# Kernel optimization log

Measured on AMD Instinct MI355X. Metric: run time of the kernel, lower is better.

## Reference

```python
import jax, jax.numpy as jnp
import numpy as np

N_GENES = 2048   # col_dim: nodes of the PPI graph, feature dim of cols-SAGE
N_CELLS = 4096   # row_dim: nodes of the KNN graph, feature dim of rows-SAGE
E_KNN = 61440
E_PPI = 65536
INTER = 512
EMBD = 128
SLOPE = 0.01       # LeakyReLU default negative_slope
SCALE_PARAM = 3.0  # cols_encoder custom attention scale

_PARAM_SHAPES = [
    ("c0_wl", (N_GENES, N_GENES)), ("c0_wr", (N_GENES, N_GENES)), ("c0_b", (N_GENES,)),
    ("r0_wl", (N_CELLS, N_CELLS)), ("r0_wr", (N_CELLS, N_CELLS)), ("r0_b", (N_CELLS,)),
    ("c1_wl", (N_GENES, N_GENES)), ("c1_wr", (N_GENES, N_GENES)), ("c1_b", (N_GENES,)),
    ("r1_wl", (N_CELLS, N_CELLS)), ("r1_wr", (N_CELLS, N_CELLS)), ("r1_b", (N_CELLS,)),
    ("gr_w", (N_CELLS, INTER)), ("gr_b", (INTER,)),
    ("tr_wq", (INTER, EMBD)), ("tr_bq", (EMBD,)), ("tr_wk", (INTER, EMBD)), ("tr_bk", (EMBD,)),
    ("tr_wv", (INTER, EMBD)), ("tr_bv", (EMBD,)), ("tr_ws", (INTER, EMBD)), ("tr_bs", (EMBD,)),
    ("gc_w", (N_GENES, INTER)), ("gc_b", (INTER,)),
    ("tc_wq", (INTER, EMBD)), ("tc_bq", (EMBD,)), ("tc_wk", (INTER, EMBD)), ("tc_bk", (EMBD,)),
    ("tc_wv", (INTER, EMBD)), ("tc_bv", (EMBD,)), ("tc_ws", (INTER, EMBD)), ("tc_bs", (EMBD,)),
    ("d1_w", (EMBD, INTER)), ("d1_b", (INTER,)),
    ("d2_w", (INTER, INTER)), ("d2_b", (INTER,)),
    ("d3_w", (INTER, N_GENES)), ("d3_b", (N_GENES,)),
]


def setup_inputs() -> dict:
    key = jax.random.key(0)
    ki = iter(jax.random.split(key, 64))
    inp = {
        "x": jax.random.normal(next(ki), (N_GENES, N_CELLS), jnp.float32),
        "knn_edge_index": jax.random.randint(next(ki), (2, E_KNN), 0, N_CELLS, dtype=jnp.int32),
        "ppi_edge_index": jax.random.randint(next(ki), (2, E_PPI), 0, N_GENES, dtype=jnp.int32),
    }
    for name, shape in _PARAM_SHAPES:
        scale = 1.0 / float(np.sqrt(shape[0])) if len(shape) == 2 else 0.01
        inp[name] = jax.random.normal(next(ki), shape, jnp.float32) * scale
    return inp


def _leaky(x):
    return jax.nn.leaky_relu(x, SLOPE)


def _gcn(x, ei, w, b):
    # GCNConv: add self loops, symmetric D^-1/2 (A+I) D^-1/2 normalization
    n = x.shape[0]
    loop = jnp.arange(n, dtype=ei.dtype)
    src = jnp.concatenate([ei[0], loop])
    dst = jnp.concatenate([ei[1], loop])
    deg = jax.ops.segment_sum(jnp.ones(src.shape, x.dtype), dst, n)
    dinv = jnp.where(deg > 0, jax.lax.rsqrt(jnp.maximum(deg, 1.0)), 0.0)
    h = x @ w
    msg = h[src] * (dinv[src] * dinv[dst])[:, None]
    return jax.ops.segment_sum(msg, dst, n) + b


def _sage(x, ei, wl, wr, b):
    # SAGEConv: mean neighbor aggregation -> lin_l, plus root lin_r
    n = x.shape[0]
    src, dst = ei[0], ei[1]
    s = jax.ops.segment_sum(x[src], dst, n)
    cnt = jax.ops.segment_sum(jnp.ones(src.shape, x.dtype), dst, n)
    agg = s / jnp.maximum(cnt, 1.0)[:, None]
    return agg @ wl + x @ wr + b


def _tconv(x, ei, wq, bq, wk, bk, wv, bv, ws, bs, scale_param):
    # TransformerConv (heads=1). scale_param=None -> per-target softmax;
    # otherwise the custom mean/std standardization + sigmoid (TransformerConvReducrLayer).
    n, d = x.shape[0], wq.shape[1]
    q = x @ wq + bq
    k = x @ wk + bk
    v = x @ wv + bv
    src, dst = ei[0], ei[1]
    alpha = jnp.sum(q[dst] * k[src], axis=-1) / jnp.sqrt(jnp.asarray(d, x.dtype))
    if scale_param is None:
        m = jax.ops.segment_max(alpha, dst, n)
        e = jnp.exp(alpha - m[dst])
        z = jax.ops.segment_sum(e, dst, n)
        a = e / jnp.where(z > 0, z, 1.0)[dst]
    else:
        mu = jnp.mean(alpha)
        sd = jnp.std(alpha, ddof=1)  # torch.std is unbiased
        a = jax.nn.sigmoid((alpha - mu) / ((1.0 / scale_param) * sd))
    out = jax.ops.segment_sum(a[:, None] * v[src], dst, n)
    return out + x @ ws + bs  # root skip (lin_skip)


def reference(x, knn_edge_index, ppi_edge_index,
              c0_wl, c0_wr, c0_b, r0_wl, r0_wr, r0_b,
              c1_wl, c1_wr, c1_b, r1_wl, r1_wr, r1_b,
              gr_w, gr_b, tr_wq, tr_bq, tr_wk, tr_bk, tr_wv, tr_bv, tr_ws, tr_bs,
              gc_w, gc_b, tc_wq, tc_bq, tc_wk, tc_bk, tc_wv, tc_bv, tc_ws, tc_bs,
              d1_w, d1_b, d2_w, d2_b, d3_w, d3_b):
    # dropout layers are identity at inference
    emb = x  # [genes, cells]
    for (cwl, cwr, cb, rwl, rwr, rb) in [
        (c0_wl, c0_wr, c0_b, r0_wl, r0_wr, r0_b),
        (c1_wl, c1_wr, c1_b, r1_wl, r1_wr, r1_b),
    ]:
        emb = _leaky(_sage(emb.T, knn_edge_index, cwl, cwr, cb)).T  # cells graph
        emb = _leaky(_sage(emb, ppi_edge_index, rwl, rwr, rb))      # genes graph
    # rows encoder: GCN + TransformerConv (softmax attention) over PPI graph
    hr = _leaky(_gcn(emb, ppi_edge_index, gr_w, gr_b))
    emb_rows = _tconv(hr, ppi_edge_index, tr_wq, tr_bq, tr_wk, tr_bk,
                      tr_wv, tr_bv, tr_ws, tr_bs, None)
    # cols encoder: GCN + reducer TransformerConv (sigmoid-standardized attention) over KNN graph
    hc = _leaky(_gcn(emb.T, knn_edge_index, gc_w, gc_b))
    emb_cols = _tconv(hc, knn_edge_index, tc_wq, tc_bq, tc_wk, tc_bk,
                      tc_wv, tc_bv, tc_ws, tc_bs, SCALE_PARAM)
    # feature decoder MLP
    h = jax.nn.relu(emb_cols @ d1_w + d1_b)
    h = jax.nn.relu(h @ d2_w + d2_b)
    out_features = h @ d3_w + d3_b
    return (emb_rows, emb_cols, out_features)
```

## Files before the change

kernel.cpp:

```cpp
#include <hip/hip_runtime.h>
#include <math.h>

#define NG 2048
#define NC 4096
#define EKNN 61440
#define EPPI 65536
#define NJMAX 14

typedef __attribute__((ext_vector_type(8))) short short8v;
typedef __attribute__((ext_vector_type(4))) float f32x4;
typedef unsigned short ushort_t;

static inline int cdiv(int a, int b) { return (a + b - 1) / b; }

__device__ __forceinline__ unsigned short f2b(float f) {
    union { float f; unsigned int i; } v; v.f = f;
    unsigned int r = v.i + 0x7FFFu + ((v.i >> 16) & 1u);
    return (unsigned short)(r >> 16);
}
__device__ __forceinline__ float bl(unsigned int u) { union { unsigned int i; float f; } v; v.i = u << 16; return v.f; }
__device__ __forceinline__ float bh(unsigned int u) { union { unsigned int i; float f; } v; v.i = u & 0xFFFF0000u; return v.f; }
__device__ __forceinline__ unsigned int pk2(float a, float b) { return (unsigned int)f2b(a) | ((unsigned int)f2b(b) << 16); }

__device__ __forceinline__ int xcd_swz_id() {
    const int nwg = gridDim.x * gridDim.y;
    const int orig = blockIdx.y * gridDim.x + blockIdx.x;
    const int q = nwg >> 3, r = nwg & 7;
    const int xcd = orig & 7, off = orig >> 3;
    return (xcd < r ? xcd * (q + 1) : r * (q + 1) + (xcd - r) * q) + off;
}

#define GLOAD_LDS16(gp, lp) __builtin_amdgcn_global_load_lds( \
    (const __attribute__((address_space(1))) void*)(gp),      \
    (__attribute__((address_space(3))) void*)(lp), 16, 0, 0)

struct TJobs {
    const void* in[NJMAX];
    ushort_t* out[NJMAX];
    int R[NJMAX], C[NJMAX], start[NJMAX], type[NJMAX];
    int n;
    int nGather;
};

template<int ACT, bool BIAS, bool OBF>
__global__ __launch_bounds__(256)
void gemm_bf16(const ushort_t* __restrict__ A,
               const ushort_t* __restrict__ Bt,
               const float* __restrict__ bias,
               float* __restrict__ Cf, ushort_t* __restrict__ Cb,
               int M, int N, int K) {
    __shared__ ushort_t lds[2][2][128 * 32];
    const int tid = threadIdx.x;
    const int lane = tid & 63, wv = tid >> 6;
    const int wm = wv >> 1, wn = wv & 1;
    const int swzid = xcd_swz_id();
    const int bm = (swzid / gridDim.x) << 7, bn = (swzid % gridDim.x) << 7;

    const ushort_t* gA = A + (size_t)bm * K;
    const ushort_t* gB = Bt + (size_t)bn * K;
    const int rsub = lane >> 2;
    const int qsw  = (lane & 3) ^ ((lane >> 3) & 3);
    const int KT = K >> 5;

    f32x4 acc[4][4];
    #pragma unroll
    for (int i = 0; i < 4; ++i)
        #pragma unroll
        for (int j = 0; j < 4; ++j) acc[i][j] = (f32x4){0.f, 0.f, 0.f, 0.f};

    auto stage = [&](int buf, int k0) {
        #pragma unroll
        for (int t = 0; t < 2; ++t) {
            const int br = (wv * 2 + t) * 16;
            GLOAD_LDS16(gA + (size_t)(br + rsub) * K + k0 + qsw * 8, &lds[buf][0][br * 32]);
            GLOAD_LDS16(gB + (size_t)(br + rsub) * K + k0 + qsw * 8, &lds[buf][1][br * 32]);
        }
    };
    const int rl = lane & 15, kg = lane >> 4;
    const int swr = (kg ^ ((rl >> 1) & 3)) * 8;

    stage(0, 0);
    int buf = 0;
    for (int kt = 0; kt < KT; ++kt) {
        __syncthreads();
        if (kt + 1 < KT) stage(buf ^ 1, (kt + 1) << 5);
        short8v a[4], b[4];
        #pragma unroll
        for (int mi = 0; mi < 4; ++mi)
            a[mi] = *(const short8v*)&lds[buf][0][(wm * 64 + mi * 16 + rl) * 32 + swr];
        #pragma unroll
        for (int ni = 0; ni < 4; ++ni)
            b[ni] = *(const short8v*)&lds[buf][1][(wn * 64 + ni * 16 + rl) * 32 + swr];
        #pragma unroll
        for (int mi = 0; mi < 4; ++mi)
            #pragma unroll
            for (int ni = 0; ni < 4; ++ni)
                acc[mi][ni] = __builtin_amdgcn_mfma_f32_16x16x32_bf16(a[mi], b[ni], acc[mi][ni], 0, 0, 0);
        buf ^= 1;
    }
    const int colL = lane & 15, rq = lane >> 4;
    #pragma unroll
    for (int mi = 0; mi < 4; ++mi) {
        const int row0 = bm + wm * 64 + mi * 16 + rq * 4;
        #pragma unroll
        for (int ni = 0; ni < 4; ++ni) {
            const int col = bn + wn * 64 + ni * 16 + colL;
            float bv = 0.f;
            if (BIAS) bv = bias[col];
            #pragma unroll
            for (int r = 0; r < 4; ++r) {
                const size_t off = (size_t)(row0 + r) * N + col;
                float v = acc[mi][ni][r];
                if (BIAS) v += bv;
                if (ACT == 2) v = fmaxf(v, 0.f);
                if (OBF) Cb[off] = f2b(v); else Cf[off] = v;
            }
        }
    }
}

template<bool BIAS, bool OBF>
__global__ __launch_bounds__(256)
void gemm2_bf16(const ushort_t* __restrict__ A0, const ushort_t* __restrict__ Bt0,
                const float* __restrict__ bias0, float* __restrict__ Cf0, ushort_t* __restrict__ Cb0,
                int N0, int K0, int nx0, int nb0,
                const ushort_t* __restrict__ A1, const ushort_t* __restrict__ Bt1,
                const float* __restrict__ bias1, float* __restrict__ Cf1, ushort_t* __restrict__ Cb1,
                int N1, int K1, int nx1) {
    __shared__ ushort_t lds[2][2][128 * 32];
    const int bid = blockIdx.x;
    const bool p1 = bid >= nb0;
    const int lbid = p1 ? bid - nb0 : bid;
    const ushort_t* A = p1 ? A1 : A0;
    const ushort_t* Bt = p1 ? Bt1 : Bt0;
    const float* bias = p1 ? bias1 : bias0;
    float* Cf = p1 ? Cf1 : Cf0;
    ushort_t* Cb = p1 ? Cb1 : Cb0;
    const int N = p1 ? N1 : N0;
    const int K = p1 ? K1 : K0;
    const int nx = p1 ? nx1 : nx0;
    const int bn = (lbid % nx) << 7, bm = (lbid / nx) << 7;

    const int tid = threadIdx.x;
    const int lane = tid & 63, wv = tid >> 6;
    const int wm = wv >> 1, wn = wv & 1;
    const ushort_t* gA = A + (size_t)bm * K;
    const ushort_t* gB = Bt + (size_t)bn * K;
    const int rsub = lane >> 2;
    const int qsw  = (lane & 3) ^ ((lane >> 3) & 3);
    const int KT = K >> 5;

    f32x4 acc[4][4];
    #pragma unroll
    for (int i = 0; i < 4; ++i)
        #pragma unroll
        for (int j = 0; j < 4; ++j) acc[i][j] = (f32x4){0.f, 0.f, 0.f, 0.f};

    auto stage = [&](int buf, int k0) {
        #pragma unroll
        for (int t = 0; t < 2; ++t) {
            const int br = (wv * 2 + t) * 16;
            GLOAD_LDS16(gA + (size_t)(br + rsub) * K + k0 + qsw * 8, &lds[buf][0][br * 32]);
            GLOAD_LDS16(gB + (size_t)(br + rsub) * K + k0 + qsw * 8, &lds[buf][1][br * 32]);
        }
    };
    const int rl = lane & 15, kg = lane >> 4;
    const int swr = (kg ^ ((rl >> 1) & 3)) * 8;

    stage(0, 0);
    int buf = 0;
    for (int kt = 0; kt < KT; ++kt) {
        __syncthreads();
        if (kt + 1 < KT) stage(buf ^ 1, (kt + 1) << 5);
        short8v a[4], b[4];
        #pragma unroll
        for (int mi = 0; mi < 4; ++mi)
            a[mi] = *(const short8v*)&lds[buf][0][(wm * 64 + mi * 16 + rl) * 32 + swr];
        #pragma unroll
        for (int ni = 0; ni < 4; ++ni)
            b[ni] = *(const short8v*)&lds[buf][1][(wn * 64 + ni * 16 + rl) * 32 + swr];
        #pragma unroll
        for (int mi = 0; mi < 4; ++mi)
            #pragma unroll
            for (int ni = 0; ni < 4; ++ni)
                acc[mi][ni] = __builtin_amdgcn_mfma_f32_16x16x32_bf16(a[mi], b[ni], acc[mi][ni], 0, 0, 0);
        buf ^= 1;
    }
    const int colL = lane & 15, rq = lane >> 4;
    #pragma unroll
    for (int mi = 0; mi < 4; ++mi) {
        const int row0 = bm + wm * 64 + mi * 16 + rq * 4;
        #pragma unroll
        for (int ni = 0; ni < 4; ++ni) {
            const int col = bn + wn * 64 + ni * 16 + colL;
            float bv = 0.f;
            if (BIAS) bv = bias[col];
            #pragma unroll
            for (int r = 0; r < 4; ++r) {
                const size_t off = (size_t)(row0 + r) * N + col;
                float v = acc[mi][ni][r];
                if (BIAS) v += bv;
                if (OBF) Cb[off] = f2b(v); else Cf[off] = v;
            }
        }
    }
}

__global__ __launch_bounds__(256)
void gemm_sage(const ushort_t* __restrict__ A0, const ushort_t* __restrict__ B0t,
               const ushort_t* __restrict__ A1, const ushort_t* __restrict__ B1t,
               const float* __restrict__ bias, ushort_t* __restrict__ Cb,
               int M, int N, int K) {
    __shared__ ushort_t lds[2][2][128 * 32];
    const int tid = threadIdx.x;
    const int lane = tid & 63, wv = tid >> 6;
    const int wm = wv >> 1, wn = wv & 1;
    const int swzid = xcd_swz_id();
    const int bm = (swzid / gridDim.x) << 7, bn = (swzid % gridDim.x) << 7;

    const ushort_t* gA0 = A0 + (size_t)bm * K;
    const ushort_t* gB0 = B0t + (size_t)bn * K;
    const ushort_t* gA1 = A1 + (size_t)bm * K;
    const ushort_t* gB1 = B1t + (size_t)bn * K;
    const int rsub = lane >> 2;
    const int qsw  = (lane & 3) ^ ((lane >> 3) & 3);
    const int KT = K >> 5;

    f32x4 acc[4][4];
    #pragma unroll
    for (int i = 0; i < 4; ++i)
        #pragma unroll
        for (int j = 0; j < 4; ++j) acc[i][j] = (f32x4){0.f, 0.f, 0.f, 0.f};

    auto stage = [&](int buf, int kt) {
        const int half = kt >= KT;
        const int k0 = (half ? (kt - KT) : kt) << 5;
        const ushort_t* sA = half ? gA1 : gA0;
        const ushort_t* sB = half ? gB1 : gB0;
        #pragma unroll
        for (int t = 0; t < 2; ++t) {
            const int br = (wv * 2 + t) * 16;
            GLOAD_LDS16(sA + (size_t)(br + rsub) * K + k0 + qsw * 8, &lds[buf][0][br * 32]);
            GLOAD_LDS16(sB + (size_t)(br + rsub) * K + k0 + qsw * 8, &lds[buf][1][br * 32]);
        }
    };
    const int rl = lane & 15, kg = lane >> 4;
    const int swr = (kg ^ ((rl >> 1) & 3)) * 8;

    stage(0, 0);
    int buf = 0;
    const int KT2 = KT * 2;
    for (int kt = 0; kt < KT2; ++kt) {
        __syncthreads();
        if (kt + 1 < KT2) stage(buf ^ 1, kt + 1);
        short8v a[4], b[4];
        #pragma unroll
        for (int mi = 0; mi < 4; ++mi)
            a[mi] = *(const short8v*)&lds[buf][0][(wm * 64 + mi * 16 + rl) * 32 + swr];
        #pragma unroll
        for (int ni = 0; ni < 4; ++ni)
            b[ni] = *(const short8v*)&lds[buf][1][(wn * 64 + ni * 16 + rl) * 32 + swr];
        #pragma unroll
        for (int mi = 0; mi < 4; ++mi)
            #pragma unroll
            for (int ni = 0; ni < 4; ++ni)
                acc[mi][ni] = __builtin_amdgcn_mfma_f32_16x16x32_bf16(a[mi], b[ni], acc[mi][ni], 0, 0, 0);
        buf ^= 1;
    }
    const int colL = lane & 15, rq = lane >> 4;
    #pragma unroll
    for (int mi = 0; mi < 4; ++mi) {
        const int row0 = bm + wm * 64 + mi * 16 + rq * 4;
        float bz[4];
        #pragma unroll
        for (int r = 0; r < 4; ++r) bz[r] = bias[row0 + r];
        #pragma unroll
        for (int ni = 0; ni < 4; ++ni) {
            const int col = bn + wn * 64 + ni * 16 + colL;
            #pragma unroll
            for (int r = 0; r < 4; ++r) {
                float v = acc[mi][ni][r] + bz[r];
                v = v > 0.f ? v : 0.01f * v;
                Cb[(size_t)(row0 + r) * N + col] = f2b(v);
            }
        }
    }
}

template<int NS>
__global__ __launch_bounds__(256)
void gather_tr(const int* __restrict__ rowptr, const int* __restrict__ srcs,
               const ushort_t* __restrict__ x, ushort_t* __restrict__ xout,
               TJobs jobs) {
    __shared__ ushort_t shm[64 * 65];
    const int tid = threadIdx.x;
    if ((int)blockIdx.x < jobs.nGather) {
        const int F = NS * 2048;
        const int node = blockIdx.x;
        int* snb = (int*)shm;
        const int beg = rowptr[node], end = rowptr[node + 1];
        float acc[NS][8];
        #pragma unroll
        for (int s = 0; s < NS; ++s)
            #pragma unroll
            for (int j = 0; j < 8; ++j) acc[s][j] = 0.f;
        for (int c = beg; c < end; c += 256) {
            const int m = min(256, end - c);
            __syncthreads();
            if (tid < m) snb[tid] = srcs[c + tid];
            __syncthreads();
            #pragma unroll 2
            for (int i = 0; i < m; ++i) {
                const uint4* row = (const uint4*)(x + (size_t)snb[i] * F);
                #pragma unroll
                for (int s = 0; s < NS; ++s) {
                    const uint4 v = row[tid + s * 256];
                    acc[s][0] += bl(v.x); acc[s][1] += bh(v.x);
                    acc[s][2] += bl(v.y); acc[s][3] += bh(v.y);
                    acc[s][4] += bl(v.z); acc[s][5] += bh(v.z);
                    acc[s][6] += bl(v.w); acc[s][7] += bh(v.w);
                }
            }
        }
        const float inv = 1.f / fmaxf((float)(end - beg), 1.f);
        uint4* orow = (uint4*)(xout + (size_t)node * F);
        #pragma unroll
        for (int s = 0; s < NS; ++s) {
            uint4 o;
            o.x = pk2(acc[s][0] * inv, acc[s][1] * inv);
            o.y = pk2(acc[s][2] * inv, acc[s][3] * inv);
            o.z = pk2(acc[s][4] * inv, acc[s][5] * inv);
            o.w = pk2(acc[s][6] * inv, acc[s][7] * inv);
            orow[tid + s * 256] = o;
        }
        return;
    }
    int b = blockIdx.x - jobs.nGather;
    int j = 0;
    while (j + 1 < jobs.n && b >= jobs.start[j + 1]) ++j;
    const int t = b - jobs.start[j];
    const int R = jobs.R[j], C = jobs.C[j];
    const int nx = C >> 6;
    const int bx = (t % nx) << 6, by = (t / nx) << 6;
    const int tr = tid >> 4, tc = (tid & 15) << 2;
    if (jobs.type[j] == 0) {
        const float* in = (const float*)jobs.in[j];
        #pragma unroll
        for (int i = 0; i < 4; ++i) {
            const int rr = tr + i * 16;
            const float4 v = *(const float4*)(in + (size_t)(by + rr) * C + bx + tc);
            shm[rr * 65 + tc + 0] = f2b(v.x); shm[rr * 65 + tc + 1] = f2b(v.y);
            shm[rr * 65 + tc + 2] = f2b(v.z); shm[rr * 65 + tc + 3] = f2b(v.w);
        }
    } else {
        const ushort_t* in = (const ushort_t*)jobs.in[j];
        #pragma unroll
        for (int i = 0; i < 4; ++i) {
            const int rr = tr + i * 16;
            const ushort4 v = *(const ushort4*)(in + (size_t)(by + rr) * C + bx + tc);
            shm[rr * 65 + tc + 0] = v.x; shm[rr * 65 + tc + 1] = v.y;
            shm[rr * 65 + tc + 2] = v.z; shm[rr * 65 + tc + 3] = v.w;
        }
    }
    __syncthreads();
    ushort_t* out = jobs.out[j];
    #pragma unroll
    for (int i = 0; i < 4; ++i) {
        const int cc = tr + i * 16;
        ushort4 o;
        o.x = shm[(tc + 0) * 65 + cc]; o.y = shm[(tc + 1) * 65 + cc];
        o.z = shm[(tc + 2) * 65 + cc]; o.w = shm[(tc + 3) * 65 + cc];
        *(ushort4*)(out + (size_t)(bx + cc) * R + by + tc) = o;
    }
}

__global__ __launch_bounds__(256)
void transpose_f2b(const float* __restrict__ in, ushort_t* __restrict__ out, int R, int C) {
    __shared__ ushort_t t[64][65];
    const int bx = blockIdx.x << 6, by = blockIdx.y << 6;
    const int tr = threadIdx.x >> 4;
    const int tc = (threadIdx.x & 15) << 2;
    #pragma unroll
    for (int i = 0; i < 4; ++i) {
        const int rr = tr + i * 16;
        const float4 v = *(const float4*)(in + (size_t)(by + rr) * C + bx + tc);
        t[rr][tc + 0] = f2b(v.x); t[rr][tc + 1] = f2b(v.y);
        t[rr][tc + 2] = f2b(v.z); t[rr][tc + 3] = f2b(v.w);
    }
    __syncthreads();
    #pragma unroll
    for (int i = 0; i < 4; ++i) {
        const int cc = tr + i * 16;
        ushort4 o;
        o.x = t[tc + 0][cc]; o.y = t[tc + 1][cc];
        o.z = t[tc + 2][cc]; o.w = t[tc + 3][cc];
        *(ushort4*)(out + (size_t)(bx + cc) * R + by + tc) = o;
    }
}

__global__ void count_dst2(const int* __restrict__ pdst, float* __restrict__ cntp,
                           const int* __restrict__ kdst, float* __restrict__ cntk) {
    int e = blockIdx.x * blockDim.x + threadIdx.x;
    if (e < EPPI) atomicAdd(&cntp[pdst[e]], 1.0f);
    else if (e < EPPI + EKNN) atomicAdd(&cntk[kdst[e - EPPI]], 1.0f);
}

__global__ void make_dinv2(const float* __restrict__ cntp, float* __restrict__ dinvp,
                           const float* __restrict__ cntk, float* __restrict__ dinvk) {
    int i = blockIdx.x * blockDim.x + threadIdx.x;
    if (i < NG) dinvp[i] = rsqrtf(cntp[i] + 1.0f);
    else if (i < NG + NC) dinvk[i - NG] = rsqrtf(cntk[i - NG] + 1.0f);
}

__global__ __launch_bounds__(256)
void scan_rowptr2(const float* __restrict__ cntp, int* __restrict__ rpp,
                  const float* __restrict__ cntk, int* __restrict__ rpk) {
    const float* cnt = blockIdx.x ? cntk : cntp;
    int* rowptr = blockIdx.x ? rpk : rpp;
    const int n = blockIdx.x ? NC : NG;
    __shared__ int part[257];
    const int tid = threadIdx.x;
    const int per = n >> 8;
    const int base = tid * per;
    int s = 0;
    for (int i = 0; i < per; ++i) s += (int)cnt[base + i];
    part[tid + 1] = s;
    if (tid == 0) part[0] = 0;
    __syncthreads();
    if (tid == 0)
        for (int i = 1; i <= 256; ++i) part[i] += part[i - 1];
    __syncthreads();
    int run = part[tid];
    for (int i = 0; i < per; ++i) {
        rowptr[base + i] = run;
        run += (int)cnt[base + i];
    }
    if (tid == 255) rowptr[n] = run;
}

__global__ void fill_csr2(const int* __restrict__ psrc, const int* __restrict__ pdst,
                          const int* __restrict__ rpp, int* __restrict__ curp,
                          int* __restrict__ srcp, int* __restrict__ eidp,
                          const int* __restrict__ ksrc, const int* __restrict__ kdst,
                          const int* __restrict__ rpk, int* __restrict__ curk,
                          int* __restrict__ srck, int* __restrict__ eidk) {
    int e = blockIdx.x * blockDim.x + threadIdx.x;
    if (e < EPPI) {
        int d = pdst[e];
        int p = atomicAdd(&curp[d], 1);
        srcp[rpp[d] + p] = psrc[e];
        eidp[rpp[d] + p] = e;
    } else if (e < EPPI + EKNN) {
        int e2 = e - EPPI;
        int d = kdst[e2];
        int p = atomicAdd(&curk[d], 1);
        srck[rpk[d] + p] = ksrc[e2];
        eidk[rpk[d] + p] = e2;
    }
}

__global__ void concat8(const float* __restrict__ a, const float* __restrict__ b,
                        const float* __restrict__ c, const float* __restrict__ d,
                        const float* __restrict__ e, const float* __restrict__ f,
                        const float* __restrict__ g, const float* __restrict__ h,
                        float* __restrict__ o, double* __restrict__ stats) {
    int i = threadIdx.x + blockIdx.x * blockDim.x;
    if (i >= 1024) return;
    if (i < 4) ((unsigned int*)stats)[i] = 0u;
    const float* s;
    int j = i & 127;
    switch (i >> 7) {
        case 0: s = a; break; case 1: s = b; break; case 2: s = c; break; case 3: s = d; break;
        case 4: s = e; break; case 5: s = f; break; case 6: s = g; break; default: s = h; break;
    }
    o[i] = s[j];
}

__global__ __launch_bounds__(128)
void gcn_gather2(const int* __restrict__ rpp, const int* __restrict__ srcp,
                 const ushort_t* __restrict__ hr, const float* __restrict__ dinvp,
                 const float* __restrict__ br, ushort_t* __restrict__ outr,
                 const int* __restrict__ rpk, const int* __restrict__ srck,
                 const ushort_t* __restrict__ hc, const float* __restrict__ dinvk,
                 const float* __restrict__ bc, ushort_t* __restrict__ outc) {
    const bool cols = blockIdx.x >= NG;
    const int node = cols ? blockIdx.x - NG : blockIdx.x;
    const int tid = threadIdx.x;
    const int* rowptr = cols ? rpk : rpp;
    const int* srcs = cols ? srck : srcp;
    const ushort_t* h = cols ? hc : hr;
    const float* dinv = cols ? dinvk : dinvp;
    const float* b = cols ? bc : br;
    ushort_t* out = cols ? outc : outr;

    const int beg = rowptr[node], end = rowptr[node + 1];
    __shared__ int snb[128];
    __shared__ float sdi[128];
    float ax = 0.f, ay = 0.f, az = 0.f, aw = 0.f;
    for (int c = beg; c < end; c += 128) {
        const int m = min(128, end - c);
        __syncthreads();
        if (tid < m) { int s = srcs[c + tid]; snb[tid] = s; sdi[tid] = dinv[s]; }
        __syncthreads();
        for (int i = 0; i < m; ++i) {
            const uint2 v = ((const uint2*)(h + (size_t)snb[i] * 512))[tid];
            const float w = sdi[i];
            ax += bl(v.x) * w; ay += bh(v.x) * w;
            az += bl(v.y) * w; aw += bh(v.y) * w;
        }
    }
    const float dd = dinv[node];
    const uint2 hv = ((const uint2*)(h + (size_t)node * 512))[tid];
    const float4 bv = ((const float4*)b)[tid];
    float4 o;
    o.x = ax * dd + bl(hv.x) * dd * dd + bv.x;
    o.y = ay * dd + bh(hv.x) * dd * dd + bv.y;
    o.z = az * dd + bl(hv.y) * dd * dd + bv.z;
    o.w = aw * dd + bh(hv.y) * dd * dd + bv.w;
    o.x = o.x > 0.f ? o.x : 0.01f * o.x;
    o.y = o.y > 0.f ? o.y : 0.01f * o.y;
    o.z = o.z > 0.f ? o.z : 0.01f * o.z;
    o.w = o.w > 0.f ? o.w : 0.01f * o.w;
    ((uint2*)(out + (size_t)node * 512))[tid] = make_uint2(pk2(o.x, o.y), pk2(o.z, o.w));
}

__global__ __launch_bounds__(256)
void edge_dot2(const int* __restrict__ psrc, const int* __restrict__ pdst,
               const float* __restrict__ qr, float* __restrict__ alphap,
               const int* __restrict__ ksrc, const int* __restrict__ kdst,
               const float* __restrict__ qc, float* __restrict__ alphak) {
    int wid = (blockIdx.x * blockDim.x + threadIdx.x) >> 6;
    int lane = threadIdx.x & 63;
    const float* q;
    float* out;
    int s, d, w;
    if (wid < EPPI) {
        w = wid; s = psrc[w]; d = pdst[w]; q = qr; out = alphap;
    } else if (wid < EPPI + EKNN) {
        w = wid - EPPI; s = ksrc[w]; d = kdst[w]; q = qc; out = alphak;
    } else return;
    const size_t qb = (size_t)d * 512;
    const size_t kb = (size_t)s * 512 + 128;
    float v = q[qb + lane] * q[kb + lane] + q[qb + 64 + lane] * q[kb + 64 + lane];
    #pragma unroll
    for (int off = 32; off; off >>= 1) v += __shfl_down(v, off);
    if (lane == 0) out[w] = v * 0.08838834764831845f;
}

__global__ __launch_bounds__(256)
void reduce_stats(const float* __restrict__ a, int E, double* __restrict__ stats) {
    double s = 0.0, s2 = 0.0;
    for (int i = blockIdx.x * blockDim.x + threadIdx.x; i < E; i += gridDim.x * blockDim.x) {
        double x = a[i];
        s += x; s2 += x * x;
    }
    #pragma unroll
    for (int off = 32; off; off >>= 1) {
        s += __shfl_down(s, off);
        s2 += __shfl_down(s2, off);
    }
    __shared__ double sh[4][2];
    int w = threadIdx.x >> 6;
    if ((threadIdx.x & 63) == 0) { sh[w][0] = s; sh[w][1] = s2; }
    __syncthreads();
    if (threadIdx.x == 0) {
        double t = sh[0][0] + sh[1][0] + sh[2][0] + sh[3][0];
        double t2 = sh[0][1] + sh[1][1] + sh[2][1] + sh[3][1];
        atomicAdd(&stats[0], t);
        atomicAdd(&stats[1], t2);
    }
}

__global__ __launch_bounds__(128)
void tconv2(const int* __restrict__ rpp, const int* __restrict__ srcp,
            const int* __restrict__ eidp, const float* __restrict__ alphap,
            const float* __restrict__ qr, float* __restrict__ outr,
            const int* __restrict__ rpk, const int* __restrict__ srck,
            const int* __restrict__ eidk, const float* __restrict__ alphak,
            const float* __restrict__ qc, const double* __restrict__ stats,
            float* __restrict__ outc, ushort_t* __restrict__ ob) {
    const int tid = threadIdx.x;
    __shared__ int snb[128];
    __shared__ float sa[128];
    if (blockIdx.x < NG) {
        const int node = blockIdx.x;
        const int beg = rpp[node], end = rpp[node + 1];
        float mx = -INFINITY;
        for (int c = beg; c < end; c += 128) {
            const int m = min(128, end - c);
            __syncthreads();
            if (tid < m) sa[tid] = alphap[eidp[c + tid]];
            __syncthreads();
            for (int i = 0; i < m; ++i) mx = fmaxf(mx, sa[i]);
        }
        float acc = 0.f, z = 0.f;
        for (int c = beg; c < end; c += 128) {
            const int m = min(128, end - c);
            __syncthreads();
            if (tid < m) { snb[tid] = srcp[c + tid]; sa[tid] = __expf(alphap[eidp[c + tid]] - mx); }
            __syncthreads();
            for (int i = 0; i < m; ++i) {
                z += sa[i];
                acc += sa[i] * qr[(size_t)snb[i] * 512 + 256 + tid];
            }
        }
        const float r = acc * (z > 0.f ? 1.f / z : 0.f) + qr[(size_t)node * 512 + 384 + tid];
        outr[(size_t)node * 128 + tid] = r;
    } else {
        const int node = blockIdx.x - NG;
        const int beg = rpk[node], end = rpk[node + 1];
        const double sum = stats[0], sumsq = stats[1];
        const double mu = sum / (double)EKNN;
        const double var = (sumsq - sum * sum / (double)EKNN) / (double)(EKNN - 1);
        const float sd = (float)sqrt(fmax(var, 0.0));
        const float kk = 3.0f / sd;
        const float fmu = (float)mu;
        float acc = 0.f;
        for (int c = beg; c < end; c += 128) {
            const int m = min(128, end - c);
            __syncthreads();
            if (tid < m) {
                snb[tid] = srck[c + tid];
                const float t = (alphak[eidk[c + tid]] - fmu) * kk;
                sa[tid] = 1.f / (1.f + __expf(-t));
            }
            __syncthreads();
            for (int i = 0; i < m; ++i)
                acc += sa[i] * qc[(size_t)snb[i] * 512 + 256 + tid];
        }
        const float r = acc + qc[(size_t)node * 512 + 384 + tid];
        outc[(size_t)node * 128 + tid] = r;
        ob[(size_t)node * 128 + tid] = f2b(r);
    }
}

static constexpr size_t NBIG = (size_t)NG * NC;
static constexpr size_t NBH = NBIG / 2;
static constexpr size_t OFF_B1 = 0;
static constexpr size_t OFF_B2 = NBH;
static constexpr size_t OFF_B3 = 2 * NBH;
static constexpr size_t OFF_WBF = 3 * NBH;
static constexpr size_t OFF_GRT   = OFF_WBF;
static constexpr size_t OFF_GCT   = OFF_GRT + 1048576;
static constexpr size_t OFF_WQR   = OFF_GCT + 524288;
static constexpr size_t OFF_WQC   = OFF_WQR + 131072;
static constexpr size_t OFF_D1T   = OFF_WQC + 131072;
static constexpr size_t OFF_D2T   = OFF_D1T + 32768;
static constexpr size_t OFF_D3T   = OFF_D2T + 131072;
static constexpr size_t OFF_HRB   = OFF_D3T + 524288;
static constexpr size_t OFF_HCB   = OFF_HRB + 524288;
static constexpr size_t OFF_H2B   = OFF_HCB + 1048576;
static constexpr size_t OFF_H3B   = OFF_H2B + 524288;
static constexpr size_t OFF_QKVSR = OFF_H3B + 1048576;
static constexpr size_t OFF_QKVSC = OFF_QKVSR + 1048576;
static constexpr size_t OFF_CBF   = OFF_QKVSC + 2097152;
static constexpr size_t OFF_TAIL = OFF_WBF + 2 * NBIG;
static constexpr size_t OFF_B4   = OFF_TAIL;
static constexpr size_t OFF_ALPHAP = OFF_B4 + 1024;
static constexpr size_t OFF_ALPHAK = OFF_ALPHAP + EPPI;
static constexpr size_t OFF_CNT  = OFF_ALPHAK + EKNN;
static constexpr size_t OFF_DINVP = OFF_CNT + 12288;
static constexpr size_t OFF_DINVK = OFF_DINVP + NG;
static constexpr size_t OFF_STATS = OFF_DINVK + NC;
static constexpr size_t OFF_RPP  = OFF_STATS + 16;
static constexpr size_t OFF_RPK  = OFF_RPP + 2064;
static constexpr size_t OFF_SRCP = OFF_RPK + 4112;
static constexpr size_t OFF_EIDP = OFF_SRCP + EPPI;
static constexpr size_t OFF_SRCK = OFF_EIDP + EPPI;
static constexpr size_t OFF_EIDK = OFF_SRCK + EKNN;

extern "C" void kernel_launch(void* const* d_in, const int* in_sizes, int n_in,
                              void* d_out, int out_size, void* d_ws, size_t ws_size,
                              hipStream_t stream) {
    const float* x      = (const float*)d_in[0];
    const int*   knn    = (const int*)d_in[1];
    const int*   ppi    = (const int*)d_in[2];
    const float* c0_wl = (const float*)d_in[3],  *c0_wr = (const float*)d_in[4],  *c0_b = (const float*)d_in[5];
    const float* r0_wl = (const float*)d_in[6],  *r0_wr = (const float*)d_in[7],  *r0_b = (const float*)d_in[8];
    const float* c1_wl = (const float*)d_in[9],  *c1_wr = (const float*)d_in[10], *c1_b = (const float*)d_in[11];
    const float* r1_wl = (const float*)d_in[12], *r1_wr = (const float*)d_in[13], *r1_b = (const float*)d_in[14];
    const float* gr_w  = (const float*)d_in[15], *gr_b  = (const float*)d_in[16];
    const float* tr_wq = (const float*)d_in[17], *tr_bq = (const float*)d_in[18];
    const float* tr_wk = (const float*)d_in[19], *tr_bk = (const float*)d_in[20];
    const float* tr_wv = (const float*)d_in[21], *tr_bv = (const float*)d_in[22];
    const float* tr_ws = (const float*)d_in[23], *tr_bs = (const float*)d_in[24];
    const float* gc_w  = (const float*)d_in[25], *gc_b  = (const float*)d_in[26];
    const float* tc_wq = (const float*)d_in[27], *tc_bq = (const float*)d_in[28];
    const float* tc_wk = (const float*)d_in[29], *tc_bk = (const float*)d_in[30];
    const float* tc_wv = (const float*)d_in[31], *tc_bv = (const float*)d_in[32];
    const float* tc_ws = (const float*)d_in[33], *tc_bs = (const float*)d_in[34];
    const float* d1_w  = (const float*)d_in[35], *d1_b  = (const float*)d_in[36];
    const float* d2_w  = (const float*)d_in[37], *d2_b  = (const float*)d_in[38];
    const float* d3_w  = (const float*)d_in[39], *d3_b  = (const float*)d_in[40];

    const int* knn_src = knn, *knn_dst = knn + EKNN;
    const int* ppi_src = ppi, *ppi_dst = ppi + EPPI;

    float* ws = (float*)d_ws;
    ushort_t* B1 = (ushort_t*)(ws + OFF_B1);
    ushort_t* B2 = (ushort_t*)(ws + OFF_B2);
    ushort_t* B3 = (ushort_t*)(ws + OFF_B3);
    ushort_t* WBF0 = (ushort_t*)(ws + OFF_WBF);
    ushort_t* WBF1 = WBF0 + 2 * NBIG;
    ushort_t* GRT = (ushort_t*)(ws + OFF_GRT);
    ushort_t* GCT = (ushort_t*)(ws + OFF_GCT);
    ushort_t* WQR = (ushort_t*)(ws + OFF_WQR);
    ushort_t* WQC = (ushort_t*)(ws + OFF_WQC);
    ushort_t* D1T = (ushort_t*)(ws + OFF_D1T);
    ushort_t* D2T = (ushort_t*)(ws + OFF_D2T);
    ushort_t* D3T = (ushort_t*)(ws + OFF_D3T);
    ushort_t* HRB = (ushort_t*)(ws + OFF_HRB);
    ushort_t* HCB = (ushort_t*)(ws + OFF_HCB);
    ushort_t* H2B = (ushort_t*)(ws + OFF_H2B);
    ushort_t* H3B = (ushort_t*)(ws + OFF_H3B);
    float* QKVSR = ws + OFF_QKVSR;
    float* QKVSC = ws + OFF_QKVSC;
    ushort_t* CBF = (ushort_t*)(ws + OFF_CBF);
    float* B4 = ws + OFF_B4;
    float* ALPHAP = ws + OFF_ALPHAP;
    float* ALPHAK = ws + OFF_ALPHAK;
    float* CNTP = ws + OFF_CNT;
    float* CNTK = CNTP + NG;
    float* DINVP = ws + OFF_DINVP;
    float* DINVK = ws + OFF_DINVK;
    double* STATS = (double*)(ws + OFF_STATS);
    int* CURP = (int*)(CNTK + NC);
    int* CURK = CURP + NG;
    int* RPP  = (int*)(ws + OFF_RPP);
    int* RPK  = (int*)(ws + OFF_RPK);
    int* SRCP = (int*)(ws + OFF_SRCP);
    int* EIDP = (int*)(ws + OFF_EIDP);
    int* SRCK = (int*)(ws + OFF_SRCK);
    int* EIDK = (int*)(ws + OFF_EIDK);

    float* out_rows = (float*)d_out;
    float* out_cols = out_rows + (size_t)NG * 128;
    float* out_feat = out_cols + (size_t)NC * 128;

    auto addJ = [](TJobs& J, const void* in, ushort_t* out, int R, int C, int type) {
        int k = J.n;
        int prevEnd = (k == 0) ? 0 : J.start[k - 1] + (J.C[k - 1] >> 6) * (J.R[k - 1] >> 6);
        J.in[k] = in; J.out[k] = out; J.R[k] = R; J.C[k] = C; J.type[k] = type;
        J.start[k] = prevEnd; J.n = k + 1;
    };
    auto jBlocks = [](const TJobs& J) {
        return (J.n == 0) ? 0 : J.start[J.n - 1] + (J.C[J.n - 1] >> 6) * (J.R[J.n - 1] >> 6);
    };
    auto gemm = [&](const ushort_t* Abf, const ushort_t* Wt, const float* bias,
                    float* Cf, ushort_t* Cb, int M, int N, int K, int mode) {
        dim3 g(N >> 7, M >> 7), blk(256);
        switch (mode) {
            case 2: gemm_bf16<0, true, false><<<g, blk, 0, stream>>>(Abf, Wt, bias, Cf, nullptr, M, N, K); break;
            case 3: gemm_bf16<2, true, true ><<<g, blk, 0, stream>>>(Abf, Wt, bias, nullptr, Cb, M, N, K); break;
        }
    };

    hipMemsetAsync(CNTP, 0, 12288 * 4, stream);
    count_dst2<<<cdiv(EPPI + EKNN, 256), 256, 0, stream>>>(ppi_dst, CNTP, knn_dst, CNTK);
    make_dinv2<<<cdiv(NG + NC, 256), 256, 0, stream>>>(CNTP, DINVP, CNTK, DINVK);
    scan_rowptr2<<<2, 256, 0, stream>>>(CNTP, RPP, CNTK, RPK);
    fill_csr2<<<cdiv(EPPI + EKNN, 256), 256, 0, stream>>>(ppi_src, ppi_dst, RPP, CURP, SRCP, EIDP,
                                                          knn_src, knn_dst, RPK, CURK, SRCK, EIDK);

    transpose_f2b<<<dim3(NC >> 6, NG >> 6), 256, 0, stream>>>(x, B1, NG, NC);
    const float* cwl[2] = {c0_wl, c1_wl}; const float* cwr[2] = {c0_wr, c1_wr}; const float* cbb[2] = {c0_b, c1_b};
    const float* rwl[2] = {r0_wl, r1_wl}; const float* rwr[2] = {r0_wr, r1_wr}; const float* rbb[2] = {r0_b, r1_b};
    for (int l = 0; l < 2; ++l) {
        TJobs Jc{}; Jc.n = 0; Jc.nGather = NC;
        addJ(Jc, cwl[l], WBF0, NG, NG, 0);
        addJ(Jc, cwr[l], WBF1, NG, NG, 0);
        gather_tr<1><<<NC + jBlocks(Jc), 256, 0, stream>>>(RPK, SRCK, B1, B2, Jc);
        gemm_sage<<<dim3(NC >> 7, NG >> 7), 256, 0, stream>>>(WBF0, B2, WBF1, B1, cbb[l], B3, NG, NC, NG);
        TJobs Jr{}; Jr.n = 0; Jr.nGather = NG;
        addJ(Jr, rwl[l], WBF0, NC, NC, 0);
        addJ(Jr, rwr[l], WBF1, NC, NC, 0);
        gather_tr<2><<<NG + jBlocks(Jr), 256, 0, stream>>>(RPP, SRCP, B3, B2, Jr);
        gemm_sage<<<dim3(NG >> 7, NC >> 7), 256, 0, stream>>>(WBF0, B2, WBF1, B3, rbb[l], B1, NC, NG, NC);
    }

    {
        TJobs Jp{}; Jp.n = 0; Jp.nGather = 0;
        addJ(Jp, B1, B3, NC, NG, 1);
        addJ(Jp, gr_w, GRT, NC, 512, 0);
        addJ(Jp, gc_w, GCT, NG, 512, 0);
        addJ(Jp, tr_wq, WQR + 0 * 65536, 512, 128, 0);
        addJ(Jp, tr_wk, WQR + 1 * 65536, 512, 128, 0);
        addJ(Jp, tr_wv, WQR + 2 * 65536, 512, 128, 0);
        addJ(Jp, tr_ws, WQR + 3 * 65536, 512, 128, 0);
        addJ(Jp, tc_wq, WQC + 0 * 65536, 512, 128, 0);
        addJ(Jp, tc_wk, WQC + 1 * 65536, 512, 128, 0);
        addJ(Jp, tc_wv, WQC + 2 * 65536, 512, 128, 0);
        addJ(Jp, tc_ws, WQC + 3 * 65536, 512, 128, 0);
        addJ(Jp, d1_w, D1T, 128, 512, 0);
        addJ(Jp, d2_w, D2T, 512, 512, 0);
        addJ(Jp, d3_w, D3T, 512, NG, 0);
        gather_tr<1><<<jBlocks(Jp), 256, 0, stream>>>(RPK, SRCK, B1, B2, Jp);
    }

    gemm2_bf16<false, true><<<64 + 128, 256, 0, stream>>>(
        B3, GRT, nullptr, nullptr, HRB, 512, NC, 4, 64,
        B1, GCT, nullptr, nullptr, HCB, 512, NG, 4);
    gcn_gather2<<<NG + NC, 128, 0, stream>>>(RPP, SRCP, HRB, DINVP, gr_b, H2B,
                                             RPK, SRCK, HCB, DINVK, gc_b, H3B);
    concat8<<<4, 256, 0, stream>>>(tr_bq, tr_bk, tr_bv, tr_bs, tc_bq, tc_bk, tc_bv, tc_bs, B4, STATS);
    gemm2_bf16<true, false><<<64 + 128, 256, 0, stream>>>(
        H2B, WQR, B4, QKVSR, nullptr, 512, 512, 4, 64,
        H3B, WQC, B4 + 512, QKVSC, nullptr, 512, 512, 4);
    edge_dot2<<<cdiv((EPPI + EKNN) * 64, 256), 256, 0, stream>>>(
        ppi_src, ppi_dst, QKVSR, ALPHAP, knn_src, knn_dst, QKVSC, ALPHAK);
    reduce_stats<<<256, 256, 0, stream>>>(ALPHAK, EKNN, STATS);
    tconv2<<<NG + NC, 128, 0, stream>>>(RPP, SRCP, EIDP, ALPHAP, QKVSR, out_rows,
                                        RPK, SRCK, EIDK, ALPHAK, QKVSC, STATS, out_cols, CBF);

    gemm(CBF, D1T, d1_b, nullptr, H2B, NC, 512, 128, 3);
    gemm(H2B, D2T, d2_b, nullptr, H3B, NC, 512, 512, 3);
    gemm(H3B, D3T, d3_b, out_feat, nullptr, NC, NG, 512, 2);

    (void)in_sizes; (void)n_in; (void)out_size; (void)ws_size;
}
```

Baseline: 943.7 us.

## Build deterministic CSR via chunked counts, fuse x transpose, narrow edge dot

Replaces atomic-order CSR fill with per-chunk destination counts, a prefix over chunks, and in-block rank computation, so edge order within each row becomes deterministic. The x transpose is folded into the same launch as the CSR fill, and degree/dinv computation merges into the chunk-prefix kernel. edge_dot2 now processes four edges per wavefront with float4 loads, and the alpha statistics use per-block partials instead of double atomics. In exchange it needs a memset of about 1.5M ints, a serial 256-step prefix per node, and an O(256) rank loop per edge.

```diff
diff --git a/kernel.cpp b/kernel.cpp
--- a/kernel.cpp
+++ b/kernel.cpp
@@ -6,6 +6,8 @@
 #define EKNN 61440
 #define EPPI 65536
 #define NJMAX 14
+#define NCH_P 256
+#define NCH_K 240
 
 typedef __attribute__((ext_vector_type(8))) short short8v;
 typedef __attribute__((ext_vector_type(4))) float f32x4;
@@ -374,42 +376,43 @@
     }
 }
 
+__global__ void cnt_chunks(const int* __restrict__ pdst, int* __restrict__ chp,
+                           const int* __restrict__ kdst, int* __restrict__ chk) {
+    const int bid = blockIdx.x, tid = threadIdx.x;
+    if (bid < NCH_P) {
+        atomicAdd(&chp[bid * NG + pdst[bid * 256 + tid]], 1);
+    } else {
+        const int c = bid - NCH_P;
+        atomicAdd(&chk[c * NC + kdst[c * 256 + tid]], 1);
+    }
+}
+
 __global__ __launch_bounds__(256)
-void transpose_f2b(const float* __restrict__ in, ushort_t* __restrict__ out, int R, int C) {
-    __shared__ ushort_t t[64][65];
-    const int bx = blockIdx.x << 6, by = blockIdx.y << 6;
-    const int tr = threadIdx.x >> 4;
-    const int tc = (threadIdx.x & 15) << 2;
-    #pragma unroll
-    for (int i = 0; i < 4; ++i) {
-        const int rr = tr + i * 16;
-        const float4 v = *(const float4*)(in + (size_t)(by + rr) * C + bx + tc);
-        t[rr][tc + 0] = f2b(v.x); t[rr][tc + 1] = f2b(v.y);
-        t[rr][tc + 2] = f2b(v.z); t[rr][tc + 3] = f2b(v.w);
-    }
-    __syncthreads();
-    #pragma unroll
-    for (int i = 0; i < 4; ++i) {
-        const int cc = tr + i * 16;
-        ushort4 o;
-        o.x = t[tc + 0][cc]; o.y = t[tc + 1][cc];
-        o.z = t[tc + 2][cc]; o.w = t[tc + 3][cc];
-        *(ushort4*)(out + (size_t)(bx + cc) * R + by + tc) = o;
-    }
-}
-
-__global__ void count_dst2(const int* __restrict__ pdst, float* __restrict__ cntp,
-                           const int* __restrict__ kdst, float* __restrict__ cntk) {
-    int e = blockIdx.x * blockDim.x + threadIdx.x;
-    if (e < EPPI) atomicAdd(&cntp[pdst[e]], 1.0f);
-    else if (e < EPPI + EKNN) atomicAdd(&cntk[kdst[e - EPPI]], 1.0f);
-}
-
-__global__ void make_dinv2(const float* __restrict__ cntp, float* __restrict__ dinvp,
-                           const float* __restrict__ cntk, float* __restrict__ dinvk) {
-    int i = blockIdx.x * blockDim.x + threadIdx.x;
-    if (i < NG) dinvp[i] = rsqrtf(cntp[i] + 1.0f);
-    else if (i < NG + NC) dinvk[i - NG] = rsqrtf(cntk[i - NG] + 1.0f);
+void pref_chunks(int* __restrict__ chp, int* __restrict__ chk,
+                 float* __restrict__ cntp, float* __restrict__ cntk,
+                 float* __restrict__ dinvp, float* __restrict__ dinvk) {
+    const int bid = blockIdx.x, tid = threadIdx.x;
+    if (bid < 8) {
+        const int d = bid * 256 + tid;
+        int run = 0;
+        for (int c = 0; c < NCH_P; ++c) {
+            const int t = chp[c * NG + d];
+            chp[c * NG + d] = run;
+            run += t;
+        }
+        cntp[d] = (float)run;
+        dinvp[d] = rsqrtf((float)run + 1.0f);
+    } else {
+        const int d = (bid - 8) * 256 + tid;
+        int run = 0;
+        for (int c = 0; c < NCH_K; ++c) {
+            const int t = chk[c * NC + d];
+            chk[c * NC + d] = run;
+            run += t;
+        }
+        cntk[d] = (float)run;
+        dinvk[d] = rsqrtf((float)run + 1.0f);
+    }
 }
 
 __global__ __launch_bounds__(256)
@@ -438,24 +441,51 @@
     if (tid == 255) rowptr[n] = run;
 }
 
-__global__ void fill_csr2(const int* __restrict__ psrc, const int* __restrict__ pdst,
-                          const int* __restrict__ rpp, int* __restrict__ curp,
-                          int* __restrict__ srcp, int* __restrict__ eidp,
-                          const int* __restrict__ ksrc, const int* __restrict__ kdst,
-                          const int* __restrict__ rpk, int* __restrict__ curk,
-                          int* __restrict__ srck, int* __restrict__ eidk) {
-    int e = blockIdx.x * blockDim.x + threadIdx.x;
-    if (e < EPPI) {
-        int d = pdst[e];
-        int p = atomicAdd(&curp[d], 1);
-        srcp[rpp[d] + p] = psrc[e];
-        eidp[rpp[d] + p] = e;
-    } else if (e < EPPI + EKNN) {
-        int e2 = e - EPPI;
-        int d = kdst[e2];
-        int p = atomicAdd(&curk[d], 1);
-        srck[rpk[d] + p] = ksrc[e2];
-        eidk[rpk[d] + p] = e2;
+__global__ __launch_bounds__(256)
+void fill_det_xt(const int* __restrict__ psrc, const int* __restrict__ pdst,
+                 const int* __restrict__ rpp, const int* __restrict__ chp,
+                 int* __restrict__ srcp, int* __restrict__ eidp,
+                 const int* __restrict__ ksrc, const int* __restrict__ kdst,
+                 const int* __restrict__ rpk, const int* __restrict__ chk,
+                 int* __restrict__ srck, int* __restrict__ eidk,
+                 const float* __restrict__ x, ushort_t* __restrict__ xt) {
+    __shared__ ushort_t shm[64 * 65];
+    const int bid = blockIdx.x, tid = threadIdx.x;
+    if (bid < NCH_P + NCH_K) {
+        int* sd = (int*)shm;
+        const bool knn = bid >= NCH_P;
+        const int c = knn ? bid - NCH_P : bid;
+        const int e = c * 256 + tid;
+        const int d = knn ? kdst[e] : pdst[e];
+        sd[tid] = d;
+        __syncthreads();
+        int rank = 0;
+        for (int j = 0; j < 256; ++j)
+            rank += (j < tid && sd[j] == d) ? 1 : 0;
+        const int slot = (knn ? rpk : rpp)[d] + (knn ? chk + c * NC : chp + c * NG)[d] + rank;
+        if (knn) { srck[slot] = ksrc[e]; eidk[slot] = e; }
+        else     { srcp[slot] = psrc[e]; eidp[slot] = e; }
+        return;
+    }
+    const int t = bid - (NCH_P + NCH_K);
+    const int bx = (t & 63) << 6;
+    const int by = (t >> 6) << 6;
+    const int tr = tid >> 4, tc = (tid & 15) << 2;
+    #pragma unroll
+    for (int i = 0; i < 4; ++i) {
+        const int rr = tr + i * 16;
+        const float4 v = *(const float4*)(x + (size_t)(by + rr) * NC + bx + tc);
+        shm[rr * 65 + tc + 0] = f2b(v.x); shm[rr * 65 + tc + 1] = f2b(v.y);
+        shm[rr * 65 + tc + 2] = f2b(v.z); shm[rr * 65 + tc + 3] = f2b(v.w);
+    }
+    __syncthreads();
+    #pragma unroll
+    for (int i = 0; i < 4; ++i) {
+        const int cc = tr + i * 16;
+        ushort4 o;
+        o.x = shm[(tc + 0) * 65 + cc]; o.y = shm[(tc + 1) * 65 + cc];
+        o.z = shm[(tc + 2) * 65 + cc]; o.w = shm[(tc + 3) * 65 + cc];
+        *(ushort4*)(xt + (size_t)(bx + cc) * NG + by + tc) = o;
     }
 }
 
@@ -463,10 +493,9 @@
                         const float* __restrict__ c, const float* __restrict__ d,
                         const float* __restrict__ e, const float* __restrict__ f,
                         const float* __restrict__ g, const float* __restrict__ h,
-                        float* __restrict__ o, double* __restrict__ stats) {
+                        float* __restrict__ o) {
     int i = threadIdx.x + blockIdx.x * blockDim.x;
     if (i >= 1024) return;
-    if (i < 4) ((unsigned int*)stats)[i] = 0u;
     const float* s;
     int j = i & 127;
     switch (i >> 7) {
@@ -529,30 +558,35 @@
                const float* __restrict__ qr, float* __restrict__ alphap,
                const int* __restrict__ ksrc, const int* __restrict__ kdst,
                const float* __restrict__ qc, float* __restrict__ alphak) {
-    int wid = (blockIdx.x * blockDim.x + threadIdx.x) >> 6;
-    int lane = threadIdx.x & 63;
+    const int gid = blockIdx.x * blockDim.x + threadIdx.x;
+    const int wid = gid >> 6;
+    const int lane = threadIdx.x & 63;
+    const int e = wid * 4 + (lane >> 4);
+    const int sub = lane & 15;
     const float* q;
     float* out;
     int s, d, w;
-    if (wid < EPPI) {
-        w = wid; s = psrc[w]; d = pdst[w]; q = qr; out = alphap;
-    } else if (wid < EPPI + EKNN) {
-        w = wid - EPPI; s = ksrc[w]; d = kdst[w]; q = qc; out = alphak;
+    if (e < EPPI) {
+        w = e; s = psrc[w]; d = pdst[w]; q = qr; out = alphap;
+    } else if (e < EPPI + EKNN) {
+        w = e - EPPI; s = ksrc[w]; d = kdst[w]; q = qc; out = alphak;
     } else return;
-    const size_t qb = (size_t)d * 512;
-    const size_t kb = (size_t)s * 512 + 128;
-    float v = q[qb + lane] * q[kb + lane] + q[qb + 64 + lane] * q[kb + 64 + lane];
-    #pragma unroll
-    for (int off = 32; off; off >>= 1) v += __shfl_down(v, off);
-    if (lane == 0) out[w] = v * 0.08838834764831845f;
+    const float4* qa = (const float4*)(q + (size_t)d * 512 + sub * 8);
+    const float4* ka = (const float4*)(q + (size_t)s * 512 + 128 + sub * 8);
+    const float4 a0 = qa[0], a1 = qa[1], b0 = ka[0], b1 = ka[1];
+    float v = a0.x * b0.x + a0.y * b0.y + a0.z * b0.z + a0.w * b0.w
+            + a1.x * b1.x + a1.y * b1.y + a1.z * b1.z + a1.w * b1.w;
+    v += __shfl_down(v, 8); v += __shfl_down(v, 4);
+    v += __shfl_down(v, 2); v += __shfl_down(v, 1);
+    if (sub == 0) out[w] = v * 0.08838834764831845f;
 }
 
 __global__ __launch_bounds__(256)
-void reduce_stats(const float* __restrict__ a, int E, double* __restrict__ stats) {
+void reduce_stats2(const float* __restrict__ a, double* __restrict__ part) {
     double s = 0.0, s2 = 0.0;
-    for (int i = blockIdx.x * blockDim.x + threadIdx.x; i < E; i += gridDim.x * blockDim.x) {
-        double x = a[i];
-        s += x; s2 += x * x;
+    for (int i = blockIdx.x * blockDim.x + threadIdx.x; i < EKNN; i += gridDim.x * blockDim.x) {
+        double xx = a[i];
+        s += xx; s2 += xx * xx;
     }
     #pragma unroll
     for (int off = 32; off; off >>= 1) {
@@ -564,10 +598,8 @@
     if ((threadIdx.x & 63) == 0) { sh[w][0] = s; sh[w][1] = s2; }
     __syncthreads();
     if (threadIdx.x == 0) {
-        double t = sh[0][0] + sh[1][0] + sh[2][0] + sh[3][0];
-        double t2 = sh[0][1] + sh[1][1] + sh[2][1] + sh[3][1];
-        atomicAdd(&stats[0], t);
-        atomicAdd(&stats[1], t2);
+        part[2 * blockIdx.x]     = sh[0][0] + sh[1][0] + sh[2][0] + sh[3][0];
+        part[2 * blockIdx.x + 1] = sh[0][1] + sh[1][1] + sh[2][1] + sh[3][1];
     }
 }
 
@@ -577,7 +609,7 @@
             const float* __restrict__ qr, float* __restrict__ outr,
             const int* __restrict__ rpk, const int* __restrict__ srck,
             const int* __restrict__ eidk, const float* __restrict__ alphak,
-            const float* __restrict__ qc, const double* __restrict__ stats,
+            const float* __restrict__ qc, const double* __restrict__ part,
             float* __restrict__ outc, ushort_t* __restrict__ ob) {
     const int tid = threadIdx.x;
     __shared__ int snb[128];
@@ -609,7 +641,8 @@
     } else {
         const int node = blockIdx.x - NG;
         const int beg = rpk[node], end = rpk[node + 1];
-        const double sum = stats[0], sumsq = stats[1];
+        double sum = 0.0, sumsq = 0.0;
+        for (int i = 0; i < 64; ++i) { sum += part[2 * i]; sumsq += part[2 * i + 1]; }
         const double mu = sum / (double)EKNN;
         const double var = (sumsq - sum * sum / (double)EKNN) / (double)(EKNN - 1);
         const float sd = (float)sqrt(fmax(var, 0.0));
@@ -661,13 +694,15 @@
 static constexpr size_t OFF_CNT  = OFF_ALPHAK + EKNN;
 static constexpr size_t OFF_DINVP = OFF_CNT + 12288;
 static constexpr size_t OFF_DINVK = OFF_DINVP + NG;
-static constexpr size_t OFF_STATS = OFF_DINVK + NC;
-static constexpr size_t OFF_RPP  = OFF_STATS + 16;
+static constexpr size_t OFF_PART = OFF_DINVK + NC;
+static constexpr size_t OFF_RPP  = OFF_PART + 256;
 static constexpr size_t OFF_RPK  = OFF_RPP + 2064;
 static constexpr size_t OFF_SRCP = OFF_RPK + 4112;
 static constexpr size_t OFF_EIDP = OFF_SRCP + EPPI;
 static constexpr size_t OFF_SRCK = OFF_EIDP + EPPI;
 static constexpr size_t OFF_EIDK = OFF_SRCK + EKNN;
+static constexpr size_t OFF_CHP  = OFF_EIDK + EKNN;
+static constexpr size_t OFF_CHK  = OFF_CHP + (size_t)NCH_P * NG;
 
 extern "C" void kernel_launch(void* const* d_in, const int* in_sizes, int n_in,
                               void* d_out, int out_size, void* d_ws, size_t ws_size,
@@ -723,15 +758,15 @@
     float* CNTK = CNTP + NG;
     float* DINVP = ws + OFF_DINVP;
     float* DINVK = ws + OFF_DINVK;
-    double* STATS = (double*)(ws + OFF_STATS);
-    int* CURP = (int*)(CNTK + NC);
-    int* CURK = CURP + NG;
+    double* PART = (double*)(ws + OFF_PART);
     int* RPP  = (int*)(ws + OFF_RPP);
     int* RPK  = (int*)(ws + OFF_RPK);
     int* SRCP = (int*)(ws + OFF_SRCP);
     int* EIDP = (int*)(ws + OFF_EIDP);
     int* SRCK = (int*)(ws + OFF_SRCK);
     int* EIDK = (int*)(ws + OFF_EIDK);
+    int* CHP  = (int*)(ws + OFF_CHP);
+    int* CHK  = (int*)(ws + OFF_CHK);
 
     float* out_rows = (float*)d_out;
     float* out_cols = out_rows + (size_t)NG * 128;
@@ -755,14 +790,14 @@
         }
     };
 
-    hipMemsetAsync(CNTP, 0, 12288 * 4, stream);
-    count_dst2<<<cdiv(EPPI + EKNN, 256), 256, 0, stream>>>(ppi_dst, CNTP, knn_dst, CNTK);
-    make_dinv2<<<cdiv(NG + NC, 256), 256, 0, stream>>>(CNTP, DINVP, CNTK, DINVK);
+    hipMemsetAsync(CHP, 0, ((size_t)NCH_P * NG + (size_t)NCH_K * NC) * 4, stream);
+    cnt_chunks<<<NCH_P + NCH_K, 256, 0, stream>>>(ppi_dst, CHP, knn_dst, CHK);
+    pref_chunks<<<24, 256, 0, stream>>>(CHP, CHK, CNTP, CNTK, DINVP, DINVK);
     scan_rowptr2<<<2, 256, 0, stream>>>(CNTP, RPP, CNTK, RPK);
-    fill_csr2<<<cdiv(EPPI + EKNN, 256), 256, 0, stream>>>(ppi_src, ppi_dst, RPP, CURP, SRCP, EIDP,
-                                                          knn_src, knn_dst, RPK, CURK, SRCK, EIDK);
-
-    transpose_f2b<<<dim3(NC >> 6, NG >> 6), 256, 0, stream>>>(x, B1, NG, NC);
+    fill_det_xt<<<NCH_P + NCH_K + 2048, 256, 0, stream>>>(
+        ppi_src, ppi_dst, RPP, CHP, SRCP, EIDP,
+        knn_src, knn_dst, RPK, CHK, SRCK, EIDK, x, B1);
+
     const float* cwl[2] = {c0_wl, c1_wl}; const float* cwr[2] = {c0_wr, c1_wr}; const float* cbb[2] = {c0_b, c1_b};
     const float* rwl[2] = {r0_wl, r1_wl}; const float* rwr[2] = {r0_wr, r1_wr}; const float* rbb[2] = {r0_b, r1_b};
     for (int l = 0; l < 2; ++l) {
@@ -802,15 +837,15 @@
         B1, GCT, nullptr, nullptr, HCB, 512, NG, 4);
     gcn_gather2<<<NG + NC, 128, 0, stream>>>(RPP, SRCP, HRB, DINVP, gr_b, H2B,
                                              RPK, SRCK, HCB, DINVK, gc_b, H3B);
-    concat8<<<4, 256, 0, stream>>>(tr_bq, tr_bk, tr_bv, tr_bs, tc_bq, tc_bk, tc_bv, tc_bs, B4, STATS);
+    concat8<<<4, 256, 0, stream>>>(tr_bq, tr_bk, tr_bv, tr_bs, tc_bq, tc_bk, tc_bv, tc_bs, B4);
     gemm2_bf16<true, false><<<64 + 128, 256, 0, stream>>>(
         H2B, WQR, B4, QKVSR, nullptr, 512, 512, 4, 64,
         H3B, WQC, B4 + 512, QKVSC, nullptr, 512, 512, 4);
-    edge_dot2<<<cdiv((EPPI + EKNN) * 64, 256), 256, 0, stream>>>(
+    edge_dot2<<<cdiv((EPPI + EKNN) * 16, 256), 256, 0, stream>>>(
         ppi_src, ppi_dst, QKVSR, ALPHAP, knn_src, knn_dst, QKVSC, ALPHAK);
-    reduce_stats<<<256, 256, 0, stream>>>(ALPHAK, EKNN, STATS);
+    reduce_stats2<<<64, 256, 0, stream>>>(ALPHAK, PART);
     tconv2<<<NG + NC, 128, 0, stream>>>(RPP, SRCP, EIDP, ALPHAP, QKVSR, out_rows,
-                                        RPK, SRCK, EIDK, ALPHAK, QKVSC, STATS, out_cols, CBF);
+                                        RPK, SRCK, EIDK, ALPHAK, QKVSC, PART, out_cols, CBF);
 
     gemm(CBF, D1T, d1_b, nullptr, H2B, NC, 512, 128, 3);
     gemm(H2B, D2T, d2_b, nullptr, H3B, NC, 512, 512, 3);
```

After: 915.2 us. -3.0%, faster.
